# Optimization experiments

Hardware: AMD Instinct MI355X
Metric: run time of the kernel (lower is better)

Reference implementation:

```python
import jax, jax.numpy as jnp
import numpy as np

N_HEAD, D_MODEL, D_HEAD = 16, 1024, 64
SCALE = 1.0 / (D_HEAD ** 0.5)
LN_EPS = 1e-5


def _rel_shift(x):
    # x: [b, n, i, j] -> Transformer-XL relative shift
    b, n, i, j = x.shape
    x_padded = jnp.pad(x, ((0, 0), (0, 0), (0, 0), (1, 0)))  # [b,n,i,j+1]
    x_padded = x_padded.reshape(b, n, j + 1, i)
    return x_padded[:, :, 1:, :].reshape(b, n, i, j)


def _layer_norm(x, g, b):
    mu = jnp.mean(x, axis=-1, keepdims=True)
    var = jnp.mean(jnp.square(x - mu), axis=-1, keepdims=True)
    return (x - mu) * jax.lax.rsqrt(var + LN_EPS) * g + b


def setup_inputs() -> dict:
    key = jax.random.key(0)
    ks = jax.random.split(key, 16)
    qlen, bsz = 2048, 2
    d = D_MODEL
    h = N_HEAD * D_HEAD
    s = 0.02
    inp = {
        "w": jax.random.normal(ks[0], (qlen, bsz, d), jnp.float32),
        "r": jax.random.normal(ks[1], (qlen, d), jnp.float32),
        "r_w_bias": jax.random.normal(ks[2], (N_HEAD, D_HEAD), jnp.float32) * s,
        "r_r_bias": jax.random.normal(ks[3], (N_HEAD, D_HEAD), jnp.float32) * s,
        "Wq": jax.random.normal(ks[4], (d, h), jnp.float32) * s,
        "bq": jnp.zeros((h,), jnp.float32),
        "Wk": jax.random.normal(ks[5], (d, h), jnp.float32) * s,
        "bk": jnp.zeros((h,), jnp.float32),
        "Wv": jax.random.normal(ks[6], (d, h), jnp.float32) * s,
        "bv": jnp.zeros((h,), jnp.float32),
        "Wr": jax.random.normal(ks[7], (d, h), jnp.float32) * s,
        "br": jnp.zeros((h,), jnp.float32),
        "Wo": jax.random.normal(ks[8], (h, d), jnp.float32) * s,
        "bo": jnp.zeros((d,), jnp.float32),
        "ln_g": jnp.ones((d,), jnp.float32),
        "ln_b": jnp.zeros((d,), jnp.float32),
        # causal mask: True = masked (future positions)
        "attn_mask": jnp.triu(jnp.ones((qlen, qlen), dtype=bool), k=1),
    }
    return inp


def reference(w, r, r_w_bias, r_r_bias, Wq, bq, Wk, bk, Wv, bv, Wr, br, Wo, bo, ln_g, ln_b, attn_mask):
    qlen, bsz, _ = w.shape
    rlen = r.shape[0]
    # projections (post-lnorm path: project raw w)
    q = (w @ Wq + bq).reshape(qlen, bsz, N_HEAD, D_HEAD)
    k = (w @ Wk + bk).reshape(qlen, bsz, N_HEAD, D_HEAD)
    v = (w @ Wv + bv).reshape(qlen, bsz, N_HEAD, D_HEAD)
    r_k = (r @ Wr + br).reshape(rlen, N_HEAD, D_HEAD)

    AC = jnp.einsum('ibnd,jbnd->bnij', q + r_w_bias, k)
    BD = jnp.einsum('ibnd,jnd->bnij', q + r_r_bias, r_k)
    BD = _rel_shift(BD)
    attn_score = SCALE * (AC + BD)
    attn_score = jnp.where(attn_mask[None, None, :, :], -jnp.inf, attn_score)

    attn_prob = jax.nn.softmax(attn_score, axis=3)
    attn_vec = jnp.einsum('bnij,jbnd->ibnd', attn_prob, v)
    attn_vec = attn_vec.reshape(qlen, bsz, N_HEAD * D_HEAD)
    attn_out = attn_vec @ Wo + bo
    return _layer_norm(w + attn_out, ln_g, ln_b)
```

## Files before the change

### kernel.cpp

```cpp
#include <hip/hip_runtime.h>
#include <math.h>

#define L 2048
#define BSZ 2
#define NH 16
#define DH 64
#define DM 1024
#define GK 1024
#define SCALE_F 0.125f

typedef __attribute__((ext_vector_type(8))) __bf16 bf16x8;
typedef __attribute__((ext_vector_type(4))) __bf16 bf16x4;
typedef __attribute__((ext_vector_type(4))) float f32x4;

__global__ __launch_bounds__(256)
void cast2_f32_bf16(const float* __restrict__ a, int na4,
                    const float* __restrict__ b, int nb4,
                    __bf16* __restrict__ da, __bf16* __restrict__ db_)
{
    int i = blockIdx.x * 256 + threadIdx.x;
    int stride = gridDim.x * 256;
    int tot = na4 + nb4;
    for (; i < tot; i += stride) {
        const float4* s; bf16x4* d; int idx;
        if (i < na4) { s = (const float4*)a; d = (bf16x4*)da; idx = i; }
        else         { s = (const float4*)b; d = (bf16x4*)db_; idx = i - na4; }
        float4 v = s[idx];
        bf16x4 o = { (__bf16)v.x, (__bf16)v.y, (__bf16)v.z, (__bf16)v.w };
        d[idx] = o;
    }
}

__global__ __launch_bounds__(256)
void transpose_w5(const float* s0, const float* s1, const float* s2,
                  const float* s3, const float* s4,
                  __bf16* d0, __bf16* d1, __bf16* d2, __bf16* d3, __bf16* d4)
{
    const float* srcs[5] = { s0, s1, s2, s3, s4 };
    __bf16*      dsts[5] = { d0, d1, d2, d3, d4 };
    const float* src = srcs[blockIdx.z];
    __bf16*      dst = dsts[blockIdx.z];
    __shared__ float tile[32][33];
    const int tx = threadIdx.x & 31, ty = threadIdx.x >> 5;
    const int x0 = blockIdx.x * 32, y0 = blockIdx.y * 32;
    #pragma unroll
    for (int i = 0; i < 32; i += 8)
        tile[ty + i][tx] = src[(size_t)(y0 + ty + i) * 1024 + x0 + tx];
    __syncthreads();
    #pragma unroll
    for (int i = 0; i < 32; i += 8)
        dst[(size_t)(x0 + ty + i) * 1024 + y0 + tx] = (__bf16)tile[tx][ty + i];
}

__global__ __launch_bounds__(256)
void gemm_bf16(const __bf16* __restrict__ A0, const __bf16* __restrict__ A1,
               const __bf16* __restrict__ B0, const __bf16* __restrict__ B1,
               int sched,
               __bf16* __restrict__ o0, __bf16* __restrict__ o1,
               __bf16* __restrict__ o2, __bf16* __restrict__ o3,
               __bf16* __restrict__ o4,
               const float* __restrict__ b0, const float* __restrict__ b1,
               const float* __restrict__ b2, const float* __restrict__ b3,
               const float* __restrict__ rwbf, const float* __restrict__ rrbf,
               float* __restrict__ of)
{
    __shared__ __bf16 As[128 * 64];
    __shared__ __bf16 Bs[128 * 64];

    const __bf16 *A, *Bt;
    int mode, bm, bn;
    if (sched == 0) {
        int id = blockIdx.x;
        if (id < 768) { A = A0; Bt = B0; mode = 0; bm = (id & 31) * 128; bn = (id >> 5) * 128; }
        else { id -= 768; A = A1; Bt = B1; mode = 1; bm = (id & 15) * 128; bn = (id >> 4) * 128; }
    } else {
        A = A0; Bt = B0; mode = 2; bm = blockIdx.x * 128; bn = blockIdx.y * 128;
    }

    const int t    = threadIdx.x;
    const int w    = t >> 6;
    const int lane = t & 63;
    const int row16 = lane & 15;
    const int kgrp  = lane >> 4;
    const int wr = w >> 1, wc = w & 1;

    f32x4 acc[4][4];
    #pragma unroll
    for (int mi = 0; mi < 4; ++mi)
        #pragma unroll
        for (int ni = 0; ni < 4; ++ni)
            acc[mi][ni] = (f32x4){0.f, 0.f, 0.f, 0.f};

    for (int k0 = 0; k0 < GK; k0 += 64) {
        __syncthreads();
        #pragma unroll
        for (int it = 0; it < 4; ++it) {
            const int lin = (it * 256 + t) * 16;
            const int row = lin >> 7;
            const int kb  = lin & 127;
            const char* ga = (const char*)(A + (size_t)(bm + row) * GK + k0) + kb;
            __builtin_amdgcn_global_load_lds(
                (const __attribute__((address_space(1))) void*)ga,
                (__attribute__((address_space(3))) void*)((char*)As + lin), 16, 0, 0);
            const char* gb = (const char*)(Bt + (size_t)(bn + row) * GK + k0) + kb;
            __builtin_amdgcn_global_load_lds(
                (const __attribute__((address_space(1))) void*)gb,
                (__attribute__((address_space(3))) void*)((char*)Bs + lin), 16, 0, 0);
        }
        __syncthreads();

        #pragma unroll
        for (int ks = 0; ks < 2; ++ks) {
            bf16x8 af[4], bfr[4];
            #pragma unroll
            for (int mi = 0; mi < 4; ++mi)
                af[mi] = *reinterpret_cast<const bf16x8*>(
                    &As[(wr * 64 + mi * 16 + row16) * 64 + kgrp * 8 + ks * 32]);
            #pragma unroll
            for (int ni = 0; ni < 4; ++ni)
                bfr[ni] = *reinterpret_cast<const bf16x8*>(
                    &Bs[(wc * 64 + ni * 16 + row16) * 64 + kgrp * 8 + ks * 32]);
            #pragma unroll
            for (int mi = 0; mi < 4; ++mi)
                #pragma unroll
                for (int ni = 0; ni < 4; ++ni)
                    acc[mi][ni] = __builtin_amdgcn_mfma_f32_16x16x32_bf16(
                        af[mi], bfr[ni], acc[mi][ni], 0, 0, 0);
        }
    }

    #pragma unroll
    for (int mi = 0; mi < 4; ++mi) {
        #pragma unroll
        for (int ni = 0; ni < 4; ++ni) {
            #pragma unroll
            for (int r = 0; r < 4; ++r) {
                const int row = bm + wr * 64 + mi * 16 + kgrp * 4 + r;
                const int col = bn + wc * 64 + ni * 16 + row16;
                const float val = acc[mi][ni][r];
                if (mode == 0) {
                    const int which = col >> 10, c = col & 1023;
                    const int n = c >> 6, dh = c & 63;
                    const int i = row >> 1, b = row & 1;
                    const size_t idx = (((size_t)(b * NH + n) * L) + i) * DH + dh;
                    if (which == 0) {
                        const float v0 = val + b0[c];
                        o0[idx] = (__bf16)(v0 + rwbf[c]);
                        o1[idx] = (__bf16)(v0 + rrbf[c]);
                    } else if (which == 1) {
                        o2[idx] = (__bf16)(val + b1[c]);
                    } else {
                        o3[idx] = (__bf16)(val + b2[c]);
                    }
                } else if (mode == 1) {
                    const int n = col >> 6, dh = col & 63;
                    o4[((size_t)n * L + row) * DH + dh] = (__bf16)(val + b3[col]);
                } else {
                    of[(size_t)row * DM + col] = val + b0[col];
                }
            }
        }
    }
}

__global__ __launch_bounds__(256, 4)
void attn_mfma(const __bf16* __restrict__ qwg, const __bf16* __restrict__ qrg,
               const __bf16* __restrict__ kg,  const __bf16* __restrict__ vg,
               const __bf16* __restrict__ rkg, __bf16* __restrict__ av_out)
{
    __shared__ __bf16 kt [64][72];
    __shared__ __bf16 vtT[64][72];
    __shared__ __bf16 pt [4][16][72];

    const int t    = threadIdx.x;
    const int w    = t >> 6;
    const int lane = t & 63;
    const int row16 = lane & 15;
    const int kgrp  = lane >> 4;

    const int bh = blockIdx.y;
    const int n  = bh & (NH - 1);
    const int b  = bh >> 4;
    const int i0 = (gridDim.x - 1 - blockIdx.x) * 64;
    const int i0w = i0 + w * 16;

    const __bf16* qwb = qwg + (size_t)bh * L * DH;
    const __bf16* qrb = qrg + (size_t)bh * L * DH;
    const __bf16* kb  = kg  + (size_t)bh * L * DH;
    const __bf16* vb  = vg  + (size_t)bh * L * DH;
    const __bf16* rkb = rkg + (size_t)n  * L * DH;

    bf16x8 qwf[2], qrf[2];
    #pragma unroll
    for (int ks = 0; ks < 2; ++ks) {
        size_t off = (size_t)(i0w + row16) * DH + kgrp * 8 + ks * 32;
        qwf[ks] = *reinterpret_cast<const bf16x8*>(qwb + off);
        qrf[ks] = *reinterpret_cast<const bf16x8*>(qrb + off);
    }

    float l_run[4] = {0.f, 0.f, 0.f, 0.f};
    f32x4 O[4];
    #pragma unroll
    for (int cb = 0; cb < 4; ++cb) O[cb] = (f32x4){0.f, 0.f, 0.f, 0.f};

    for (int j0 = 0; j0 <= i0 + 63; j0 += 64) {
        __syncthreads();

        {
            int j  = t >> 2;
            int d0 = (t & 3) * 16;
            bf16x8 ka  = *reinterpret_cast<const bf16x8*>(kb + (size_t)(j0 + j) * DH + d0);
            bf16x8 kb2 = *reinterpret_cast<const bf16x8*>(kb + (size_t)(j0 + j) * DH + d0 + 8);
            *reinterpret_cast<bf16x8*>(&kt[j][d0])     = ka;
            *reinterpret_cast<bf16x8*>(&kt[j][d0 + 8]) = kb2;
            bf16x8 va  = *reinterpret_cast<const bf16x8*>(vb + (size_t)(j0 + j) * DH + d0);
            bf16x8 vb2 = *reinterpret_cast<const bf16x8*>(vb + (size_t)(j0 + j) * DH + d0 + 8);
            #pragma unroll
            for (int kk = 0; kk < 8; ++kk) {
                vtT[d0 + kk][j]     = va[kk];
                vtT[d0 + 8 + kk][j] = vb2[kk];
            }
        }
        __syncthreads();

        f32x4 ac[4];
        #pragma unroll
        for (int cb = 0; cb < 4; ++cb) ac[cb] = (f32x4){0.f, 0.f, 0.f, 0.f};
        #pragma unroll
        for (int ks = 0; ks < 2; ++ks)
            #pragma unroll
            for (int cb = 0; cb < 4; ++cb) {
                bf16x8 kf = *reinterpret_cast<const bf16x8*>(&kt[16 * cb + row16][kgrp * 8 + ks * 32]);
                ac[cb] = __builtin_amdgcn_mfma_f32_16x16x32_bf16(qwf[ks], kf, ac[cb], 0, 0, 0);
            }

        f32x4 db[5];
        #pragma unroll
        for (int cb = 0; cb < 5; ++cb) db[cb] = (f32x4){0.f, 0.f, 0.f, 0.f};
        const int pw0 = (L - 1) + j0 - (i0w + 15);
        #pragma unroll
        for (int ks = 0; ks < 2; ++ks)
            #pragma unroll
            for (int cb = 0; cb < 5; ++cb) {
                int p = pw0 + 16 * cb + row16;
                p = p > (L - 1) ? (L - 1) : p;
                bf16x8 rf = *reinterpret_cast<const bf16x8*>(
                    rkb + (size_t)p * DH + kgrp * 8 + ks * 32);
                db[cb] = __builtin_amdgcn_mfma_f32_16x16x32_bf16(qrf[ks], rf, db[cb], 0, 0, 0);
            }

        #pragma unroll
        for (int r = 0; r < 4; ++r) {
            const int ri = kgrp * 4 + r;
            const int i_glob = i0w + ri;
            const int u  = row16 + 15 - ri;
            const int lo = u & 15;
            const int hi = u >> 4;
            const int srclane = (lane & 48) | lo;
            float T[5];
            #pragma unroll
            for (int c2 = 0; c2 < 5; ++c2)
                T[c2] = __shfl(db[c2][r], srclane, 64);
            float rsum = 0.f;
            #pragma unroll
            for (int cb = 0; cb < 4; ++cb) {
                const int jj = 16 * cb + row16;
                float bd = hi ? T[cb + 1] : T[cb];
                float s = SCALE_F * (ac[cb][r] + bd);
                if (j0 + jj > i_glob) s = -INFINITY;
                float p = __expf(s);
                pt[w][ri][jj] = (__bf16)p;
                rsum += p;
            }
            #pragma unroll
            for (int off = 1; off < 16; off <<= 1)
                rsum += __shfl_xor(rsum, off);
            l_run[r] += rsum;
        }

        #pragma unroll
        for (int ks = 0; ks < 2; ++ks) {
            bf16x8 pf = *reinterpret_cast<const bf16x8*>(&pt[w][row16][kgrp * 8 + ks * 32]);
            #pragma unroll
            for (int cb = 0; cb < 4; ++cb) {
                bf16x8 vf = *reinterpret_cast<const bf16x8*>(&vtT[16 * cb + row16][kgrp * 8 + ks * 32]);
                O[cb] = __builtin_amdgcn_mfma_f32_16x16x32_bf16(pf, vf, O[cb], 0, 0, 0);
            }
        }
    }

    #pragma unroll
    for (int r = 0; r < 4; ++r) {
        const int i_glob = i0w + kgrp * 4 + r;
        const float inv = 1.0f / l_run[r];
        #pragma unroll
        for (int cb = 0; cb < 4; ++cb) {
            av_out[(size_t)(i_glob * BSZ + b) * (NH * DH) + n * DH + 16 * cb + row16] =
                (__bf16)(O[cb][r] * inv);
        }
    }
}

__global__ __launch_bounds__(256)
void ln_fused(const float* __restrict__ w, const float* __restrict__ ao,
              const float* __restrict__ g, const float* __restrict__ bb,
              float* __restrict__ out)
{
    const int row = blockIdx.x;
    const float* wr = w  + (size_t)row * DM;
    const float* ar = ao + (size_t)row * DM;
    const int t = threadIdx.x;
    float x[4];
    float s = 0.f;
    #pragma unroll
    for (int j = 0; j < 4; ++j) {
        int c = t + j * 256;
        x[j] = wr[c] + ar[c];
        s += x[j];
    }
    __shared__ float red[4];
    #pragma unroll
    for (int off = 1; off < 64; off <<= 1) s += __shfl_xor(s, off);
    int wid = t >> 6, lane = t & 63;
    if (lane == 0) red[wid] = s;
    __syncthreads();
    float mu = (red[0] + red[1] + red[2] + red[3]) * (1.0f / DM);
    float ss = 0.f;
    #pragma unroll
    for (int j = 0; j < 4; ++j) { float d = x[j] - mu; ss += d * d; }
    #pragma unroll
    for (int off = 1; off < 64; off <<= 1) ss += __shfl_xor(ss, off);
    __syncthreads();
    if (lane == 0) red[wid] = ss;
    __syncthreads();
    float var = (red[0] + red[1] + red[2] + red[3]) * (1.0f / DM);
    float rstd = rsqrtf(var + 1e-5f);
    #pragma unroll
    for (int j = 0; j < 4; ++j) {
        int c = t + j * 256;
        out[(size_t)row * DM + c] = (x[j] - mu) * rstd * g[c] + bb[c];
    }
}

extern "C" void kernel_launch(void* const* d_in, const int* in_sizes, int n_in,
                              void* d_out, int out_size, void* d_ws, size_t ws_size,
                              hipStream_t stream)
{
    (void)in_sizes; (void)n_in; (void)out_size; (void)ws_size;
    const float* w   = (const float*)d_in[0];
    const float* r   = (const float*)d_in[1];
    const float* rwb = (const float*)d_in[2];
    const float* rrb = (const float*)d_in[3];
    const float* Wq  = (const float*)d_in[4];
    const float* bq  = (const float*)d_in[5];
    const float* Wk  = (const float*)d_in[6];
    const float* bk  = (const float*)d_in[7];
    const float* Wv  = (const float*)d_in[8];
    const float* bv  = (const float*)d_in[9];
    const float* Wr  = (const float*)d_in[10];
    const float* br  = (const float*)d_in[11];
    const float* Wo  = (const float*)d_in[12];
    const float* bo  = (const float*)d_in[13];
    const float* lng = (const float*)d_in[14];
    const float* lnb = (const float*)d_in[15];
    float* out = (float*)d_out;

    const size_t NQ = (size_t)BSZ * NH * L * DH;
    char* wsb = (char*)d_ws;
    __bf16* w_bf    = (__bf16*)wsb;  wsb += (size_t)2 * L * DM * 2;
    __bf16* r_bf    = (__bf16*)wsb;  wsb += (size_t)L * DM * 2;
    __bf16* wqkv_t  = (__bf16*)wsb;  wsb += (size_t)3 * DM * DM * 2;
    __bf16* wr_t    = (__bf16*)wsb;  wsb += (size_t)DM * DM * 2;
    __bf16* wo_t    = (__bf16*)wsb;  wsb += (size_t)DM * DM * 2;
    __bf16* qw_ws   = (__bf16*)wsb;  wsb += NQ * 2;
    __bf16* qr_ws   = (__bf16*)wsb;  wsb += NQ * 2;
    __bf16* k_ws    = (__bf16*)wsb;  wsb += NQ * 2;
    __bf16* v_ws    = (__bf16*)wsb;  wsb += NQ * 2;
    __bf16* rk_ws   = (__bf16*)wsb;  wsb += (size_t)NH * L * DH * 2;
    __bf16* av_ws   = (__bf16*)wsb;  wsb += NQ * 2;
    float*  ao_ws   = (float*)wsb;

    dim3 blk(256);
    cast2_f32_bf16<<<dim3(1536), blk, 0, stream>>>(
        w, (2 * L * DM) / 4, r, (L * DM) / 4, w_bf, r_bf);
    transpose_w5<<<dim3(32, 32, 5), blk, 0, stream>>>(
        Wq, Wk, Wv, Wr, Wo,
        wqkv_t, wqkv_t + (size_t)DM * DM, wqkv_t + (size_t)2 * DM * DM, wr_t, wo_t);

    gemm_bf16<<<dim3(896), blk, 0, stream>>>(w_bf, r_bf, wqkv_t, wr_t, 0,
        qw_ws, qr_ws, k_ws, v_ws, rk_ws, bq, bk, bv, br, rwb, rrb, nullptr);

    attn_mfma<<<dim3(L / 64, BSZ * NH), blk, 0, stream>>>(qw_ws, qr_ws, k_ws, v_ws, rk_ws, av_ws);

    gemm_bf16<<<dim3(32, 8), blk, 0, stream>>>(av_ws, nullptr, wo_t, nullptr, 1,
        nullptr, nullptr, nullptr, nullptr, nullptr, bo, nullptr, nullptr, nullptr,
        nullptr, nullptr, ao_ws);

    ln_fused<<<dim3(L * BSZ), blk, 0, stream>>>(w, ao_ws, lng, lnb, out);
}
```

Before: 508.7 us.

## Split attention across key chunks with atomic partial accumulation and a reduce pass

Causal attention work is redistributed so each block handles one query tile and at most a 512-key chunk. This balances the triangular workload and raises the number of blocks. Unnormalized output partials and row sums are accumulated into a zeroed fp32 buffer with atomicAdd. A separate reduce kernel then normalizes and writes bf16. This adds a memset, an extra launch and atomic traffic, and it relies on the partials sharing a common exponent reference.

```diff
diff --git a/kernel.cpp b/kernel.cpp
--- a/kernel.cpp
+++ b/kernel.cpp
@@ -8,6 +8,8 @@
 #define DM 1024
 #define GK 1024
 #define SCALE_F 0.125f
+
+#define PSLOT 4160
 
 typedef __attribute__((ext_vector_type(8))) __bf16 bf16x8;
 typedef __attribute__((ext_vector_type(4))) __bf16 bf16x4;
@@ -164,13 +166,20 @@
 }
 
 __global__ __launch_bounds__(256, 4)
-void attn_mfma(const __bf16* __restrict__ qwg, const __bf16* __restrict__ qrg,
-               const __bf16* __restrict__ kg,  const __bf16* __restrict__ vg,
-               const __bf16* __restrict__ rkg, __bf16* __restrict__ av_out)
+void attn_partial(const __bf16* __restrict__ qwg, const __bf16* __restrict__ qrg,
+                  const __bf16* __restrict__ kg,  const __bf16* __restrict__ vg,
+                  const __bf16* __restrict__ rkg, float* __restrict__ P)
 {
     __shared__ __bf16 kt [64][72];
     __shared__ __bf16 vtT[64][72];
     __shared__ __bf16 pt [4][16][72];
+
+    int x = blockIdx.x;
+    int it, jc;
+    if (x < 8)       { it = x;                      jc = 0; }
+    else if (x < 24) { int y = x - 8;  it = 8  + (y >> 1); jc = y & 1; }
+    else if (x < 48) { int y = x - 24; it = 16 + y / 3;    jc = y - (y / 3) * 3; }
+    else             { int y = x - 48; it = 24 + (y >> 2); jc = y & 3; }
 
     const int t    = threadIdx.x;
     const int w    = t >> 6;
@@ -180,9 +189,10 @@
 
     const int bh = blockIdx.y;
     const int n  = bh & (NH - 1);
-    const int b  = bh >> 4;
-    const int i0 = (gridDim.x - 1 - blockIdx.x) * 64;
+    const int i0 = it * 64;
     const int i0w = i0 + w * 16;
+    const int jstart = jc * 512;
+    const int jend   = min(jstart + 512, i0 + 64);
 
     const __bf16* qwb = qwg + (size_t)bh * L * DH;
     const __bf16* qrb = qrg + (size_t)bh * L * DH;
@@ -203,7 +213,7 @@
     #pragma unroll
     for (int cb = 0; cb < 4; ++cb) O[cb] = (f32x4){0.f, 0.f, 0.f, 0.f};
 
-    for (int j0 = 0; j0 <= i0 + 63; j0 += 64) {
+    for (int j0 = jstart; j0 < jend; j0 += 64) {
         __syncthreads();
 
         {
@@ -289,15 +299,37 @@
         }
     }
 
+    float* Pb = P + ((size_t)bh * 32 + it) * PSLOT;
     #pragma unroll
     for (int r = 0; r < 4; ++r) {
-        const int i_glob = i0w + kgrp * 4 + r;
-        const float inv = 1.0f / l_run[r];
-        #pragma unroll
-        for (int cb = 0; cb < 4; ++cb) {
-            av_out[(size_t)(i_glob * BSZ + b) * (NH * DH) + n * DH + 16 * cb + row16] =
-                (__bf16)(O[cb][r] * inv);
-        }
+        const int row = w * 16 + kgrp * 4 + r;
+        #pragma unroll
+        for (int cb = 0; cb < 4; ++cb)
+            atomicAdd(&Pb[row * 64 + 16 * cb + row16], O[cb][r]);
+        if (row16 == 0)
+            atomicAdd(&Pb[4096 + row], l_run[r]);
+    }
+}
+
+__global__ __launch_bounds__(256)
+void attn_reduce(const float* __restrict__ P, __bf16* __restrict__ av)
+{
+    const int bh = blockIdx.y;
+    const int it = blockIdx.x;
+    const int n = bh & (NH - 1), b = bh >> 4;
+    const float* Pb = P + ((size_t)bh * 32 + it) * PSLOT;
+    const int t = threadIdx.x;
+    const int row = t >> 2;
+    const int c0 = (t & 3) * 16;
+    const float inv = 1.0f / Pb[4096 + row];
+    const int i_glob = it * 64 + row;
+    __bf16* dst = av + (size_t)(i_glob * BSZ + b) * (NH * DH) + n * DH + c0;
+    #pragma unroll
+    for (int v4 = 0; v4 < 4; ++v4) {
+        float4 o = *reinterpret_cast<const float4*>(&Pb[row * 64 + c0 + v4 * 4]);
+        bf16x4 ov = { (__bf16)(o.x * inv), (__bf16)(o.y * inv),
+                      (__bf16)(o.z * inv), (__bf16)(o.w * inv) };
+        *reinterpret_cast<bf16x4*>(dst + v4 * 4) = ov;
     }
 }
 
@@ -366,6 +398,7 @@
     float* out = (float*)d_out;
 
     const size_t NQ = (size_t)BSZ * NH * L * DH;
+    const size_t PN = (size_t)BSZ * NH * 32 * PSLOT;
     char* wsb = (char*)d_ws;
     __bf16* w_bf    = (__bf16*)wsb;  wsb += (size_t)2 * L * DM * 2;
     __bf16* r_bf    = (__bf16*)wsb;  wsb += (size_t)L * DM * 2;
@@ -378,9 +411,12 @@
     __bf16* v_ws    = (__bf16*)wsb;  wsb += NQ * 2;
     __bf16* rk_ws   = (__bf16*)wsb;  wsb += (size_t)NH * L * DH * 2;
     __bf16* av_ws   = (__bf16*)wsb;  wsb += NQ * 2;
-    float*  ao_ws   = (float*)wsb;
+    float*  P_ws    = (float*)wsb;
+    float*  ao_ws   = P_ws;
 
     dim3 blk(256);
+    hipMemsetAsync(P_ws, 0, PN * sizeof(float), stream);
+
     cast2_f32_bf16<<<dim3(1536), blk, 0, stream>>>(
         w, (2 * L * DM) / 4, r, (L * DM) / 4, w_bf, r_bf);
     transpose_w5<<<dim3(32, 32, 5), blk, 0, stream>>>(
@@ -390,7 +426,9 @@
     gemm_bf16<<<dim3(896), blk, 0, stream>>>(w_bf, r_bf, wqkv_t, wr_t, 0,
         qw_ws, qr_ws, k_ws, v_ws, rk_ws, bq, bk, bv, br, rwb, rrb, nullptr);
 
-    attn_mfma<<<dim3(L / 64, BSZ * NH), blk, 0, stream>>>(qw_ws, qr_ws, k_ws, v_ws, rk_ws, av_ws);
+    attn_partial<<<dim3(80, BSZ * NH), blk, 0, stream>>>(
+        qw_ws, qr_ws, k_ws, v_ws, rk_ws, P_ws);
+    attn_reduce<<<dim3(32, BSZ * NH), blk, 0, stream>>>(P_ws, av_ws);
 
     gemm_bf16<<<dim3(32, 8), blk, 0, stream>>>(av_ws, nullptr, wo_t, nullptr, 1,
         nullptr, nullptr, nullptr, nullptr, nullptr, bo, nullptr, nullptr, nullptr,
```

After: 421.4 us. -17.2%, faster.

## Double-buffer K/V tiles, pre-transpose V, and widen attention blocks to 128 rows

Applied to the files above, without the earlier changes.

Adds a separate kernel that transposes V into a [d][j] layout, so the attention kernel can load V tiles with vector copies instead of scalar scattered LDS writes. The attention kernel now uses 512 threads (8 waves, 128 query rows per block) and double-buffers the K/V shared tiles, prefetching the next tile into registers while computing on the current one. This drops one barrier per iteration. Waves whose rows are fully masked skip compute. The cost is an extra kernel launch and V round trip through global memory, fewer blocks (512 vs 1024), and more LDS per block, which may lower occupancy.

```diff
diff --git a/kernel.cpp b/kernel.cpp
--- a/kernel.cpp
+++ b/kernel.cpp
@@ -50,6 +50,23 @@
     #pragma unroll
     for (int i = 0; i < 32; i += 8)
         dst[(size_t)(x0 + ty + i) * 1024 + y0 + tx] = (__bf16)tile[tx][ty + i];
+}
+
+__global__ __launch_bounds__(256)
+void transpose_v(const __bf16* __restrict__ src, __bf16* __restrict__ dst)
+{
+    __shared__ __bf16 tile[32][34];
+    const __bf16* s = src + (size_t)blockIdx.z * L * DH;
+    __bf16*       d = dst + (size_t)blockIdx.z * L * DH;
+    const int tx = threadIdx.x & 31, ty = threadIdx.x >> 5;
+    const int j0 = blockIdx.x * 32, d0 = blockIdx.y * 32;
+    #pragma unroll
+    for (int i = 0; i < 32; i += 8)
+        tile[ty + i][tx] = s[(size_t)(j0 + ty + i) * DH + d0 + tx];
+    __syncthreads();
+    #pragma unroll
+    for (int i = 0; i < 32; i += 8)
+        d[(size_t)(d0 + ty + i) * L + j0 + tx] = tile[tx][ty + i];
 }
 
 __global__ __launch_bounds__(256)
@@ -163,14 +180,14 @@
     }
 }
 
-__global__ __launch_bounds__(256, 4)
-void attn_mfma(const __bf16* __restrict__ qwg, const __bf16* __restrict__ qrg,
-               const __bf16* __restrict__ kg,  const __bf16* __restrict__ vg,
-               const __bf16* __restrict__ rkg, __bf16* __restrict__ av_out)
-{
-    __shared__ __bf16 kt [64][72];
-    __shared__ __bf16 vtT[64][72];
-    __shared__ __bf16 pt [4][16][72];
+__global__ __launch_bounds__(512, 4)
+void attn_fused(const __bf16* __restrict__ qwg, const __bf16* __restrict__ qrg,
+                const __bf16* __restrict__ kg,  const __bf16* __restrict__ vTg,
+                const __bf16* __restrict__ rkg, __bf16* __restrict__ av_out)
+{
+    __shared__ __bf16 kt [2][64][72];
+    __shared__ __bf16 vtT[2][64][72];
+    __shared__ __bf16 pt [8][16][72];
 
     const int t    = threadIdx.x;
     const int w    = t >> 6;
@@ -181,13 +198,15 @@
     const int bh = blockIdx.y;
     const int n  = bh & (NH - 1);
     const int b  = bh >> 4;
-    const int i0 = (gridDim.x - 1 - blockIdx.x) * 64;
+    const int it = gridDim.x - 1 - blockIdx.x;
+    const int i0 = it * 128;
     const int i0w = i0 + w * 16;
+    const int jend = i0 + 128;
 
     const __bf16* qwb = qwg + (size_t)bh * L * DH;
     const __bf16* qrb = qrg + (size_t)bh * L * DH;
     const __bf16* kb  = kg  + (size_t)bh * L * DH;
-    const __bf16* vb  = vg  + (size_t)bh * L * DH;
+    const __bf16* vTb = vTg + (size_t)bh * L * DH;
     const __bf16* rkb = rkg + (size_t)n  * L * DH;
 
     bf16x8 qwf[2], qrf[2];
@@ -198,94 +217,106 @@
         qrf[ks] = *reinterpret_cast<const bf16x8*>(qrb + off);
     }
 
+    const int sj = t >> 3;
+    const int sc = (t & 7) * 8;
+
+    {
+        bf16x8 k0v = *reinterpret_cast<const bf16x8*>(kb + (size_t)sj * DH + sc);
+        bf16x8 v0v = *reinterpret_cast<const bf16x8*>(vTb + (size_t)sj * L + sc);
+        *reinterpret_cast<bf16x8*>(&kt[0][sj][sc])  = k0v;
+        *reinterpret_cast<bf16x8*>(&vtT[0][sj][sc]) = v0v;
+    }
+    __syncthreads();
+
     float l_run[4] = {0.f, 0.f, 0.f, 0.f};
     f32x4 O[4];
     #pragma unroll
     for (int cb = 0; cb < 4; ++cb) O[cb] = (f32x4){0.f, 0.f, 0.f, 0.f};
 
-    for (int j0 = 0; j0 <= i0 + 63; j0 += 64) {
-        __syncthreads();
-
-        {
-            int j  = t >> 2;
-            int d0 = (t & 3) * 16;
-            bf16x8 ka  = *reinterpret_cast<const bf16x8*>(kb + (size_t)(j0 + j) * DH + d0);
-            bf16x8 kb2 = *reinterpret_cast<const bf16x8*>(kb + (size_t)(j0 + j) * DH + d0 + 8);
-            *reinterpret_cast<bf16x8*>(&kt[j][d0])     = ka;
-            *reinterpret_cast<bf16x8*>(&kt[j][d0 + 8]) = kb2;
-            bf16x8 va  = *reinterpret_cast<const bf16x8*>(vb + (size_t)(j0 + j) * DH + d0);
-            bf16x8 vb2 = *reinterpret_cast<const bf16x8*>(vb + (size_t)(j0 + j) * DH + d0 + 8);
-            #pragma unroll
-            for (int kk = 0; kk < 8; ++kk) {
-                vtT[d0 + kk][j]     = va[kk];
-                vtT[d0 + 8 + kk][j] = vb2[kk];
+    int cur = 0;
+    for (int j0 = 0; j0 < jend; j0 += 64) {
+        const bool more = (j0 + 64 < jend);
+
+        bf16x8 skA, svA;
+        if (more) {
+            skA = *reinterpret_cast<const bf16x8*>(kb + (size_t)(j0 + 64 + sj) * DH + sc);
+            svA = *reinterpret_cast<const bf16x8*>(vTb + (size_t)sj * L + j0 + 64 + sc);
+        }
+
+        if (j0 <= i0w + 15) {
+            f32x4 ac[4];
+            #pragma unroll
+            for (int cb = 0; cb < 4; ++cb) ac[cb] = (f32x4){0.f, 0.f, 0.f, 0.f};
+            #pragma unroll
+            for (int ks = 0; ks < 2; ++ks)
+                #pragma unroll
+                for (int cb = 0; cb < 4; ++cb) {
+                    bf16x8 kf = *reinterpret_cast<const bf16x8*>(
+                        &kt[cur][16 * cb + row16][kgrp * 8 + ks * 32]);
+                    ac[cb] = __builtin_amdgcn_mfma_f32_16x16x32_bf16(qwf[ks], kf, ac[cb], 0, 0, 0);
+                }
+
+            f32x4 db[5];
+            #pragma unroll
+            for (int cb = 0; cb < 5; ++cb) db[cb] = (f32x4){0.f, 0.f, 0.f, 0.f};
+            const int pw0 = (L - 1) + j0 - (i0w + 15);
+            #pragma unroll
+            for (int ks = 0; ks < 2; ++ks)
+                #pragma unroll
+                for (int cb = 0; cb < 5; ++cb) {
+                    int p = pw0 + 16 * cb + row16;
+                    p = p > (L - 1) ? (L - 1) : p;
+                    bf16x8 rf = *reinterpret_cast<const bf16x8*>(
+                        rkb + (size_t)p * DH + kgrp * 8 + ks * 32);
+                    db[cb] = __builtin_amdgcn_mfma_f32_16x16x32_bf16(qrf[ks], rf, db[cb], 0, 0, 0);
+                }
+
+            #pragma unroll
+            for (int r = 0; r < 4; ++r) {
+                const int ri = kgrp * 4 + r;
+                const int i_glob = i0w + ri;
+                const int u  = row16 + 15 - ri;
+                const int lo = u & 15;
+                const int hi = u >> 4;
+                const int srclane = (lane & 48) | lo;
+                float T[5];
+                #pragma unroll
+                for (int c2 = 0; c2 < 5; ++c2)
+                    T[c2] = __shfl(db[c2][r], srclane, 64);
+                float rsum = 0.f;
+                #pragma unroll
+                for (int cb = 0; cb < 4; ++cb) {
+                    const int jj = 16 * cb + row16;
+                    float bd = hi ? T[cb + 1] : T[cb];
+                    float s = SCALE_F * (ac[cb][r] + bd);
+                    if (j0 + jj > i_glob) s = -INFINITY;
+                    float p = __expf(s);
+                    pt[w][ri][jj] = (__bf16)p;
+                    rsum += p;
+                }
+                #pragma unroll
+                for (int off = 1; off < 16; off <<= 1)
+                    rsum += __shfl_xor(rsum, off);
+                l_run[r] += rsum;
             }
-        }
-        __syncthreads();
-
-        f32x4 ac[4];
-        #pragma unroll
-        for (int cb = 0; cb < 4; ++cb) ac[cb] = (f32x4){0.f, 0.f, 0.f, 0.f};
-        #pragma unroll
-        for (int ks = 0; ks < 2; ++ks)
-            #pragma unroll
-            for (int cb = 0; cb < 4; ++cb) {
-                bf16x8 kf = *reinterpret_cast<const bf16x8*>(&kt[16 * cb + row16][kgrp * 8 + ks * 32]);
-                ac[cb] = __builtin_amdgcn_mfma_f32_16x16x32_bf16(qwf[ks], kf, ac[cb], 0, 0, 0);
+
+            #pragma unroll
+            for (int ks = 0; ks < 2; ++ks) {
+                bf16x8 pf = *reinterpret_cast<const bf16x8*>(&pt[w][row16][kgrp * 8 + ks * 32]);
+                #pragma unroll
+                for (int cb = 0; cb < 4; ++cb) {
+                    bf16x8 vf = *reinterpret_cast<const bf16x8*>(
+                        &vtT[cur][16 * cb + row16][kgrp * 8 + ks * 32]);
+                    O[cb] = __builtin_amdgcn_mfma_f32_16x16x32_bf16(pf, vf, O[cb], 0, 0, 0);
+                }
             }
-
-        f32x4 db[5];
-        #pragma unroll
-        for (int cb = 0; cb < 5; ++cb) db[cb] = (f32x4){0.f, 0.f, 0.f, 0.f};
-        const int pw0 = (L - 1) + j0 - (i0w + 15);
-        #pragma unroll
-        for (int ks = 0; ks < 2; ++ks)
-            #pragma unroll
-            for (int cb = 0; cb < 5; ++cb) {
-                int p = pw0 + 16 * cb + row16;
-                p = p > (L - 1) ? (L - 1) : p;
-                bf16x8 rf = *reinterpret_cast<const bf16x8*>(
-                    rkb + (size_t)p * DH + kgrp * 8 + ks * 32);
-                db[cb] = __builtin_amdgcn_mfma_f32_16x16x32_bf16(qrf[ks], rf, db[cb], 0, 0, 0);
-            }
-
-        #pragma unroll
-        for (int r = 0; r < 4; ++r) {
-            const int ri = kgrp * 4 + r;
-            const int i_glob = i0w + ri;
-            const int u  = row16 + 15 - ri;
-            const int lo = u & 15;
-            const int hi = u >> 4;
-            const int srclane = (lane & 48) | lo;
-            float T[5];
-            #pragma unroll
-            for (int c2 = 0; c2 < 5; ++c2)
-                T[c2] = __shfl(db[c2][r], srclane, 64);
-            float rsum = 0.f;
-            #pragma unroll
-            for (int cb = 0; cb < 4; ++cb) {
-                const int jj = 16 * cb + row16;
-                float bd = hi ? T[cb + 1] : T[cb];
-                float s = SCALE_F * (ac[cb][r] + bd);
-                if (j0 + jj > i_glob) s = -INFINITY;
-                float p = __expf(s);
-                pt[w][ri][jj] = (__bf16)p;
-                rsum += p;
-            }
-            #pragma unroll
-            for (int off = 1; off < 16; off <<= 1)
-                rsum += __shfl_xor(rsum, off);
-            l_run[r] += rsum;
-        }
-
-        #pragma unroll
-        for (int ks = 0; ks < 2; ++ks) {
-            bf16x8 pf = *reinterpret_cast<const bf16x8*>(&pt[w][row16][kgrp * 8 + ks * 32]);
-            #pragma unroll
-            for (int cb = 0; cb < 4; ++cb) {
-                bf16x8 vf = *reinterpret_cast<const bf16x8*>(&vtT[16 * cb + row16][kgrp * 8 + ks * 32]);
-                O[cb] = __builtin_amdgcn_mfma_f32_16x16x32_bf16(pf, vf, O[cb], 0, 0, 0);
-            }
+        }
+
+        if (more) {
+            *reinterpret_cast<bf16x8*>(&kt[cur ^ 1][sj][sc])  = skA;
+            *reinterpret_cast<bf16x8*>(&vtT[cur ^ 1][sj][sc]) = svA;
+            __syncthreads();
+            cur ^= 1;
         }
     }
 
@@ -376,6 +407,7 @@
     __bf16* qr_ws   = (__bf16*)wsb;  wsb += NQ * 2;
     __bf16* k_ws    = (__bf16*)wsb;  wsb += NQ * 2;
     __bf16* v_ws    = (__bf16*)wsb;  wsb += NQ * 2;
+    __bf16* vT_ws   = (__bf16*)wsb;  wsb += NQ * 2;
     __bf16* rk_ws   = (__bf16*)wsb;  wsb += (size_t)NH * L * DH * 2;
     __bf16* av_ws   = (__bf16*)wsb;  wsb += NQ * 2;
     float*  ao_ws   = (float*)wsb;
@@ -390,7 +422,10 @@
     gemm_bf16<<<dim3(896), blk, 0, stream>>>(w_bf, r_bf, wqkv_t, wr_t, 0,
         qw_ws, qr_ws, k_ws, v_ws, rk_ws, bq, bk, bv, br, rwb, rrb, nullptr);
 
-    attn_mfma<<<dim3(L / 64, BSZ * NH), blk, 0, stream>>>(qw_ws, qr_ws, k_ws, v_ws, rk_ws, av_ws);
+    transpose_v<<<dim3(L / 32, DH / 32, BSZ * NH), blk, 0, stream>>>(v_ws, vT_ws);
+
+    attn_fused<<<dim3(16, BSZ * NH), dim3(512), 0, stream>>>(
+        qw_ws, qr_ws, k_ws, vT_ws, rk_ws, av_ws);
 
     gemm_bf16<<<dim3(32, 8), blk, 0, stream>>>(av_ws, nullptr, wo_t, nullptr, 1,
         nullptr, nullptr, nullptr, nullptr, nullptr, bo, nullptr, nullptr, nullptr,
```

Result: no change. 511.4 us (+0.5%).
